# Kernel optimization log

Measured on AMD Instinct MI355X. Metric: run time of the kernel, lower is better.

## Reference

```python
import jax, jax.numpy as jnp
import numpy as np

E, H = 1024, 16


def setup_inputs() -> dict:
    key = jax.random.key(0)
    k1, k2, k3, k4 = jax.random.split(key, 4)
    B, L = 4, 2048
    embeddings = jax.random.normal(k1, (B, L, E), dtype=jnp.float32)
    mask = jax.random.randint(k2, (B, L, L), 0, 2) == 1  # True = masked out
    # Params (torch Linear y = x @ W.T; we store already-transposed [in, out])
    W_qkv = jax.random.normal(k3, (E, 3 * E), dtype=jnp.float32) * 0.02
    W_out = jax.random.normal(k4, (E, E), dtype=jnp.float32) * 0.02
    return {"embeddings": embeddings, "mask": mask, "W_qkv": W_qkv, "W_out": W_out}


def reference(embeddings, mask, W_qkv, W_out):
    B, L, E_ = embeddings.shape
    A = E_ // H
    scale = A ** (-0.5)
    qkv = embeddings @ W_qkv                       # [B, L, 3E]
    qkv = qkv.reshape(B, L, H, 3 * A).transpose(0, 2, 1, 3)  # [B, H, L, 3A]
    q, k, v = jnp.split(qkv, 3, axis=-1)           # each [B, H, L, A]
    scores = jnp.einsum('bhqa,bhka->bhqk', q, k) * scale  # [B, H, L, L]
    m = mask[:, None, :, :]                        # [B, 1, L, L]
    fully = jnp.all(m, axis=-1, keepdims=True)     # rows with every key masked
    scores = jnp.where(m, -jnp.inf, scores)
    scores = jnp.where(fully, 0.0, scores)         # keep softmax finite
    attn = jax.nn.softmax(scores, axis=-1)
    attn = jnp.where(fully, 0.0, attn)             # == torch nan_to_num(0)
    values = jnp.einsum('bhqk,bhka->bhqa', attn, v)  # [B, H, L, A]
    values = values.transpose(0, 2, 1, 3).reshape(B, L, E_)
    return values @ W_out
```

## Files before the change

kernel.cpp:

```cpp
#include <hip/hip_runtime.h>
#include <hip/hip_bf16.h>

#define B_   4
#define L_   2048
#define E_   1024
#define H_   16
#define T_   8192
#define K_   1024

typedef __attribute__((ext_vector_type(8))) short bf16x8;
typedef __attribute__((ext_vector_type(4))) float f32x4;
typedef __attribute__((ext_vector_type(4))) unsigned u32x4;

#define CSC_ (0.125f * 1.44269504f)

__device__ __forceinline__ ushort f2b(float f) {
    union { float f; unsigned u; } x; x.f = f;
    unsigned r = (x.u + 0x7fffu + ((x.u >> 16) & 1u)) >> 16;
    return (ushort)r;
}

__device__ __forceinline__ float fexp2(float x) {
#if __has_builtin(__builtin_amdgcn_exp2f)
    return __builtin_amdgcn_exp2f(x);
#else
    return __expf(x * 0.69314718056f);
#endif
}

__device__ __forceinline__ unsigned pack2bf(float a, float b) {
#if __has_builtin(__builtin_amdgcn_cvt_pk_bf16_f32)
    auto t = __builtin_amdgcn_cvt_pk_bf16_f32(a, b);
    return __builtin_bit_cast(unsigned, t);
#else
    unsigned ua = __builtin_bit_cast(unsigned, a) + 0x8000u;
    unsigned ub = __builtin_bit_cast(unsigned, b) + 0x8000u;
    return __builtin_amdgcn_perm(ub, ua, 0x07060302);
#endif
}

#define GLD_LDS16(gp, lp) __builtin_amdgcn_global_load_lds( \
    (const __attribute__((address_space(1))) void*)(gp), \
    (__attribute__((address_space(3))) void*)(lp), 16, 0, 0)

__global__ void detect_mask_layout(const unsigned char* __restrict__ m, int* flag) {
    __shared__ int s;
    if (threadIdx.x == 0) s = 0;
    __syncthreads();
    int found = 0;
    for (int i = threadIdx.x; i < 4096; i += 256)
        if ((i & 3) != 0 && m[i] != 0) found = 1;
    if (found) atomicOr(&s, 1);
    __syncthreads();
    if (threadIdx.x == 0) *flag = s;
}

__global__ void pack_mask(const void* __restrict__ mraw, const int* __restrict__ flag,
                          unsigned* __restrict__ tbits) {
    int row  = blockIdx.x;
    int lane = threadIdx.x & 63;
    int wave = threadIdx.x >> 6;
    int isByte = *flag;
    int b = row >> 11, q = row & 2047;
    const unsigned char* mb = (const unsigned char*)mraw;
    const int*           mi = (const int*)mraw;
    long long base = (long long)row * L_;
    for (int w = wave; w < 32; w += 4) {
        int idx = w * 64 + lane;
        int v = isByte ? (int)mb[base + idx] : mi[base + idx];
        unsigned long long word = __ballot(v == 0);
        if (lane == 0) {
            tbits[((size_t)b * 64 + 2 * w)     * 2048 + q] = (unsigned)word;
            tbits[((size_t)b * 64 + 2 * w + 1) * 2048 + q] = (unsigned)(word >> 32);
        }
    }
}

__global__ __launch_bounds__(256) void conv_bf16(const float* __restrict__ in,
                                                 ushort* __restrict__ out) {
    int i = blockIdx.x * 256 + threadIdx.x;
    float4 v = ((const float4*)in)[i];
    uint2 o;
    o.x = (unsigned)f2b(v.x) | ((unsigned)f2b(v.y) << 16);
    o.y = (unsigned)f2b(v.z) | ((unsigned)f2b(v.w) << 16);
    ((uint2*)out)[i] = o;
}

__global__ __launch_bounds__(256) void transpose_conv(const float* __restrict__ in,
        ushort* __restrict__ out, int R, int Cn) {
    __shared__ float t[32][33];
    int c0 = blockIdx.x * 32, r0 = blockIdx.y * 32;
    int x = threadIdx.x & 31, y = threadIdx.x >> 5;
#pragma unroll
    for (int k = 0; k < 4; ++k)
        t[y + k * 8][x] = in[(size_t)(r0 + y + k * 8) * Cn + c0 + x];
    __syncthreads();
#pragma unroll
    for (int k = 0; k < 4; ++k)
        out[(size_t)(c0 + y + k * 8) * R + r0 + x] = f2b(t[x][y + k * 8]);
}

template<int NDIM, int MODE>
__global__ __launch_bounds__(256) void gemm_bf16(
        const ushort* __restrict__ Ab, const ushort* __restrict__ Bt,
        float* __restrict__ Cg, ushort* __restrict__ Qb,
        ushort* __restrict__ Kb, ushort* __restrict__ Vt) {
    __shared__ ushort As[128 * 64];
    __shared__ ushort Bs[128 * 64];
    const int tid = threadIdx.x;
    const int wv = tid >> 6, ln = tid & 63;
    const int bn = blockIdx.x * 128, bm = blockIdx.y * 128;
    const int wm = (wv & 1) * 64, wn = (wv >> 1) * 64;
    const int row16 = ln & 15, quad = ln >> 4;
    const int cg8 = (((ln & 7) ^ (ln >> 3)) * 8);

    f32x4 acc[4][4];
#pragma unroll
    for (int i = 0; i < 4; ++i)
#pragma unroll
        for (int j = 0; j < 4; ++j) acc[i][j] = (f32x4){0.f, 0.f, 0.f, 0.f};

    for (int k0 = 0; k0 < K_; k0 += 64) {
        __syncthreads();
#pragma unroll
        for (int it = 0; it < 4; ++it) {
            int rA = wv * 32 + it * 8 + (ln >> 3);
            GLD_LDS16(Ab + (size_t)(bm + rA) * K_ + k0 + cg8, &As[(wv * 32 + it * 8) * 64]);
            GLD_LDS16(Bt + (size_t)(bn + rA) * K_ + k0 + cg8, &Bs[(wv * 32 + it * 8) * 64]);
        }
        __syncthreads();
#pragma unroll
        for (int ks = 0; ks < 2; ++ks) {
            const int ch = (((ks * 4 + quad) ^ (ln & 7)) * 8);
            bf16x8 af[4], bf[4];
#pragma unroll
            for (int i = 0; i < 4; ++i)
                af[i] = *(const bf16x8*)&As[(wm + i * 16 + row16) * 64 + ch];
#pragma unroll
            for (int j = 0; j < 4; ++j)
                bf[j] = *(const bf16x8*)&Bs[(wn + j * 16 + row16) * 64 + ch];
#pragma unroll
            for (int i = 0; i < 4; ++i)
#pragma unroll
                for (int j = 0; j < 4; ++j)
                    acc[i][j] = __builtin_amdgcn_mfma_f32_16x16x32_bf16(
                        af[i], bf[j], acc[i][j], 0, 0, 0);
        }
    }

    if (MODE == 0) {
#pragma unroll
        for (int i = 0; i < 4; ++i)
#pragma unroll
            for (int j = 0; j < 4; ++j) {
                int col = bn + wn + j * 16 + row16;
#pragma unroll
                for (int r = 0; r < 4; ++r) {
                    int row = bm + wm + i * 16 + quad * 4 + r;
                    Cg[(size_t)row * NDIM + col] = acc[i][j][r];
                }
            }
    } else {
#pragma unroll
        for (int j = 0; j < 4; ++j) {
            int col = bn + wn + j * 16 + row16;
            int h = col / 192, w = col - h * 192;
            int sel = w >> 6, a = w & 63;
            float qs = (sel == 0) ? CSC_ : 1.0f;
#pragma unroll
            for (int i = 0; i < 4; ++i)
#pragma unroll
                for (int r = 0; r < 4; ++r) {
                    int rowg = bm + wm + i * 16 + quad * 4 + r;
                    int b = rowg >> 11, l = rowg & 2047;
                    ushort v = f2b(acc[i][j][r] * qs);
                    size_t bh = (size_t)(b * H_ + h);
                    if (sel == 0)      Qb[(bh * L_ + l) * 64 + a] = v;
                    else if (sel == 1) Kb[(bh * L_ + l) * 64 + a] = v;
                    else {
                        int k5 = l & 31;
                        int lp = (l & ~31) | (2 * (k5 & 15) + (k5 >> 4));
                        Vt[(bh * 64 + a) * L_ + lp] = v;
                    }
                }
        }
    }
}

__global__ __launch_bounds__(512, 4) void attn_mfma(
        const ushort* __restrict__ Qb, const ushort* __restrict__ Kb,
        const ushort* __restrict__ Vt, const unsigned* __restrict__ tbits,
        ushort* __restrict__ vals) {
    __shared__ ushort KV[6][4096];

    const int tid = threadIdx.x, wv = tid >> 6, ln = tid & 63;
    const int bh = blockIdx.x, b = bh >> 4, h = bh & 15;
    const int q0 = blockIdx.y * 128;
    const int row16 = ln & 15, quad = ln >> 4;
    const int lh = ln >> 3, ll = ln & 7;
    const int cg8 = ((ll ^ lh) * 8);

    const ushort* Kg = Kb + (size_t)bh * L_ * 64;
    const ushort* Vg = Vt + (size_t)bh * 64 * L_;

    const int wk = wv & 3;
    const bool isK = (wv < 4);
    const int vc4 = ll ^ lh;
    const ushort* vstage = Vg + (size_t)(wk * 8 + lh + 32 * (vc4 >> 2)) * L_ + (vc4 & 3) * 8;
    const ushort* kstage = Kg + (size_t)(wk * 8 + lh) * 64 + cg8;

    {
        const ushort* Qgw = Qb + ((size_t)bh * L_ + q0 + wv * 16) * 64;
        GLD_LDS16(Qgw + (size_t)lh * 64 + cg8,       &KV[0][(wv * 16) * 64]);
        GLD_LDS16(Qgw + (size_t)(8 + lh) * 64 + cg8, &KV[0][(wv * 16 + 8) * 64]);
    }
    __syncthreads();
    bf16x8 aq[2];
#pragma unroll
    for (int ks = 0; ks < 2; ++ks)
        aq[ks] = *(const bf16x8*)&KV[0][(wv * 16 + row16) * 64 +
                                        (((ks * 4 + quad) ^ (row16 & 7)) * 8)];
    __syncthreads();

    if (isK) {
        GLD_LDS16(kstage,               &KV[0][(wk * 8) * 64]);
        GLD_LDS16(kstage + 2048,        &KV[0][(32 + wk * 8) * 64]);
        GLD_LDS16(kstage + 4096,        &KV[1][(wk * 8) * 64]);
        GLD_LDS16(kstage + 4096 + 2048, &KV[1][(32 + wk * 8) * 64]);
        kstage += 8192;
    } else {
        GLD_LDS16(vstage,      &KV[3][(wk * 8) * 64]);
        GLD_LDS16(vstage + 32, &KV[3][(32 + wk * 8) * 64]);
        GLD_LDS16(vstage + 64, &KV[4][(wk * 8) * 64]);
        GLD_LDS16(vstage + 96, &KV[4][(32 + wk * 8) * 64]);
        vstage += 128;
    }

    bf16x8 vone;
#pragma unroll
    for (int i = 0; i < 8; ++i) vone[i] = (short)0x3F80;
    const f32x4 zf = (f32x4){0.f, 0.f, 0.f, 0.f};

    f32x4 oacc[4], lacc = zf;
#pragma unroll
    for (int t = 0; t < 4; ++t) oacc[t] = zf;

    const unsigned* mptr = tbits + (size_t)b * 64 * 2048 + (q0 + wv * 16 + row16);

    auto qk = [&](const ushort* kbuf, int sub, f32x4 (&s)[2]) {
        __builtin_amdgcn_s_setprio(1);
#pragma unroll
        for (int ks = 0; ks < 2; ++ks) {
            bf16x8 bk[2];
#pragma unroll
            for (int t = 0; t < 2; ++t)
                bk[t] = *(const bf16x8*)&kbuf[(sub * 32 + t * 16 + row16) * 64 +
                                              (((ks * 4 + quad) ^ (row16 & 7)) * 8)];
#pragma unroll
            for (int t = 0; t < 2; ++t)
                s[t] = __builtin_amdgcn_mfma_f32_16x16x32_bf16(
                    bk[t], aq[ks], ks ? s[t] : zf, 0, 0, 0);
        }
        __builtin_amdgcn_s_setprio(0);
    };

    auto sm_pv = [&](f32x4 (&sa)[2], unsigned m, const ushort* vbuf, int sub) {
        u32x4 pw;
#pragma unroll
        for (int r = 0; r < 4; ++r) {
            unsigned sh = m >> (quad * 4 + r);
            unsigned pk = pack2bf(fexp2(sa[0][r]), fexp2(sa[1][r]));
            pk &= (sh & 0x00010001u) * 0xFFFFu;
            pw[r] = pk;
        }
        bf16x8 ap = __builtin_bit_cast(bf16x8, pw);
        bf16x8 bv[4];
#pragma unroll
        for (int t = 0; t < 4; ++t)
            bv[t] = *(const bf16x8*)&vbuf[(sub * 32 + (t & 1) * 16 + row16) * 64 +
                                          ((((t >> 1) * 4 + quad) ^ (row16 & 7)) * 8)];
        __builtin_amdgcn_s_setprio(1);
        lacc = __builtin_amdgcn_mfma_f32_16x16x32_bf16(ap, vone, lacc, 0, 0, 0);
#pragma unroll
        for (int t = 0; t < 4; ++t)
            oacc[t] = __builtin_amdgcn_mfma_f32_16x16x32_bf16(
                ap, bv[t], oacc[t], 0, 0, 0);
        __builtin_amdgcn_s_setprio(0);
    };

    auto iter = [&](const ushort* kb, const ushort* vb,
                    ushort* kn, ushort* vn, bool st) {
        unsigned m0 = mptr[0], m1 = mptr[2048];
        mptr += 4096;
        __builtin_amdgcn_sched_barrier(0);
        if (st) {
            if (isK) {
                GLD_LDS16(kstage,        kn + (wk * 8) * 64);
                GLD_LDS16(kstage + 2048, kn + (32 + wk * 8) * 64);
                kstage += 4096;
            } else {
                GLD_LDS16(vstage,      vn + (wk * 8) * 64);
                GLD_LDS16(vstage + 32, vn + (32 + wk * 8) * 64);
                vstage += 64;
            }
        }
        f32x4 s0[2], s1[2];
        qk(kb, 0, s0);
        qk(kb, 1, s1);
        sm_pv(s0, m0, vb, 0);
        sm_pv(s1, m1, vb, 1);
        asm volatile("s_waitcnt vmcnt(2)" ::: "memory");
        __builtin_amdgcn_s_barrier();
        __builtin_amdgcn_sched_barrier(0);
    };

    asm volatile("s_waitcnt vmcnt(2)" ::: "memory");
    __builtin_amdgcn_s_barrier();
    __builtin_amdgcn_sched_barrier(0);

    for (int g = 0; g < 10; ++g) {
        iter(KV[0], KV[3], KV[2], KV[5], true);
        iter(KV[1], KV[4], KV[0], KV[3], true);
        iter(KV[2], KV[5], KV[1], KV[4], true);
    }
    iter(KV[0], KV[3], KV[2], KV[5], false);
    iter(KV[1], KV[4], KV[0], KV[3], false);

#pragma unroll
    for (int r = 0; r < 4; ++r) {
        float l = lacc[r];
        float inv = (l > 0.f) ? 1.0f / l : 0.f;
        int qrow = q0 + wv * 16 + quad * 4 + r;
        size_t base = ((size_t)b * L_ + qrow) * E_ + h * 64;
#pragma unroll
        for (int t = 0; t < 4; ++t)
            vals[base + t * 16 + row16] = f2b(oacc[t][r] * inv);
    }
}

extern "C" void kernel_launch(void* const* d_in, const int* in_sizes, int n_in,
                              void* d_out, int out_size, void* d_ws, size_t ws_size,
                              hipStream_t stream) {
    const float* emb  = (const float*)d_in[0];
    const void*  mask = d_in[1];
    const float* wqkv = (const float*)d_in[2];
    const float* wout = (const float*)d_in[3];
    float* out = (float*)d_out;

    char* ws = (char*)d_ws;
    const size_t NEED = 4096ull + 2097152ull + 2ull * 46137344ull;
    if (ws_size < NEED) return;

    int* flag = (int*)ws;
    unsigned* tbits = (unsigned*)(ws + 4096);
    ushort* embb  = (ushort*)(ws + 4096 + 2097152);
    ushort* Wqkvt = embb  + 8388608;
    ushort* Wott  = Wqkvt + 3145728;
    ushort* Qb    = Wott  + 1048576;
    ushort* Kb    = Qb    + 8388608;
    ushort* Vt    = Kb    + 8388608;
    ushort* vals  = Vt    + 8388608;

    detect_mask_layout<<<1, 256, 0, stream>>>((const unsigned char*)mask, flag);
    pack_mask<<<T_, 256, 0, stream>>>(mask, flag, tbits);
    conv_bf16<<<8192, 256, 0, stream>>>(emb, embb);
    transpose_conv<<<dim3(96, 32), 256, 0, stream>>>(wqkv, Wqkvt, 1024, 3072);
    transpose_conv<<<dim3(32, 32), 256, 0, stream>>>(wout, Wott, 1024, 1024);
    gemm_bf16<3072, 1><<<dim3(24, 64), 256, 0, stream>>>(
        embb, Wqkvt, nullptr, Qb, Kb, Vt);
    attn_mfma<<<dim3(64, 16), 512, 0, stream>>>(Qb, Kb, Vt, tbits, vals);
    gemm_bf16<1024, 0><<<dim3(8, 64), 256, 0, stream>>>(
        vals, Wott, out, nullptr, nullptr, nullptr);
}
```

Measured before the change: 355.6 us.

## Process two 16-row query groups per wave to reuse K/V fragments

```diff
diff --git a/kernel.cpp b/kernel.cpp
--- a/kernel.cpp
+++ b/kernel.cpp
@@ -195,7 +195,7 @@
 
     const int tid = threadIdx.x, wv = tid >> 6, ln = tid & 63;
     const int bh = blockIdx.x, b = bh >> 4, h = bh & 15;
-    const int q0 = blockIdx.y * 128;
+    const int q0 = blockIdx.y * 256;
     const int row16 = ln & 15, quad = ln >> 4;
     const int lh = ln >> 3, ll = ln & 7;
     const int cg8 = ((ll ^ lh) * 8);
@@ -209,17 +209,23 @@
     const ushort* vstage = Vg + (size_t)(wk * 8 + lh + 32 * (vc4 >> 2)) * L_ + (vc4 & 3) * 8;
     const ushort* kstage = Kg + (size_t)(wk * 8 + lh) * 64 + cg8;
 
+    ushort* lds = &KV[0][0];
+
     {
-        const ushort* Qgw = Qb + ((size_t)bh * L_ + q0 + wv * 16) * 64;
-        GLD_LDS16(Qgw + (size_t)lh * 64 + cg8,       &KV[0][(wv * 16) * 64]);
-        GLD_LDS16(Qgw + (size_t)(8 + lh) * 64 + cg8, &KV[0][(wv * 16 + 8) * 64]);
+        const ushort* Qgw = Qb + ((size_t)bh * L_ + q0 + wv * 32) * 64;
+#pragma unroll
+        for (int it = 0; it < 4; ++it)
+            GLD_LDS16(Qgw + (size_t)(it * 8 + lh) * 64 + cg8,
+                      lds + (wv * 32 + it * 8) * 64);
     }
     __syncthreads();
-    bf16x8 aq[2];
-#pragma unroll
-    for (int ks = 0; ks < 2; ++ks)
-        aq[ks] = *(const bf16x8*)&KV[0][(wv * 16 + row16) * 64 +
-                                        (((ks * 4 + quad) ^ (row16 & 7)) * 8)];
+    bf16x8 aq[2][2];
+#pragma unroll
+    for (int rg = 0; rg < 2; ++rg)
+#pragma unroll
+        for (int ks = 0; ks < 2; ++ks)
+            aq[rg][ks] = *(const bf16x8*)&lds[(wv * 32 + rg * 16 + row16) * 64 +
+                                              (((ks * 4 + quad) ^ (row16 & 7)) * 8)];
     __syncthreads();
 
     if (isK) {
@@ -241,13 +247,17 @@
     for (int i = 0; i < 8; ++i) vone[i] = (short)0x3F80;
     const f32x4 zf = (f32x4){0.f, 0.f, 0.f, 0.f};
 
-    f32x4 oacc[4], lacc = zf;
-#pragma unroll
-    for (int t = 0; t < 4; ++t) oacc[t] = zf;
-
-    const unsigned* mptr = tbits + (size_t)b * 64 * 2048 + (q0 + wv * 16 + row16);
-
-    auto qk = [&](const ushort* kbuf, int sub, f32x4 (&s)[2]) {
+    f32x4 oacc[2][4], lacc[2];
+#pragma unroll
+    for (int rg = 0; rg < 2; ++rg) {
+        lacc[rg] = zf;
+#pragma unroll
+        for (int t = 0; t < 4; ++t) oacc[rg][t] = zf;
+    }
+
+    const unsigned* mptr = tbits + (size_t)b * 64 * 2048 + (q0 + wv * 32 + row16);
+
+    auto qk = [&](const ushort* kbuf, int sub, f32x4 (&s)[2][2]) {
         __builtin_amdgcn_s_setprio(1);
 #pragma unroll
         for (int ks = 0; ks < 2; ++ks) {
@@ -257,40 +267,53 @@
                 bk[t] = *(const bf16x8*)&kbuf[(sub * 32 + t * 16 + row16) * 64 +
                                               (((ks * 4 + quad) ^ (row16 & 7)) * 8)];
 #pragma unroll
-            for (int t = 0; t < 2; ++t)
-                s[t] = __builtin_amdgcn_mfma_f32_16x16x32_bf16(
-                    bk[t], aq[ks], ks ? s[t] : zf, 0, 0, 0);
+            for (int rg = 0; rg < 2; ++rg)
+#pragma unroll
+                for (int t = 0; t < 2; ++t)
+                    s[rg][t] = __builtin_amdgcn_mfma_f32_16x16x32_bf16(
+                        bk[t], aq[rg][ks], ks ? s[rg][t] : zf, 0, 0, 0);
         }
         __builtin_amdgcn_s_setprio(0);
     };
 
-    auto sm_pv = [&](f32x4 (&sa)[2], unsigned m, const ushort* vbuf, int sub) {
-        u32x4 pw;
-#pragma unroll
-        for (int r = 0; r < 4; ++r) {
-            unsigned sh = m >> (quad * 4 + r);
-            unsigned pk = pack2bf(fexp2(sa[0][r]), fexp2(sa[1][r]));
-            pk &= (sh & 0x00010001u) * 0xFFFFu;
-            pw[r] = pk;
-        }
-        bf16x8 ap = __builtin_bit_cast(bf16x8, pw);
+    auto sm_pv = [&](f32x4 (&sa)[2][2], unsigned mlo, unsigned mhi,
+                     const ushort* vbuf, int sub) {
+        bf16x8 ap[2];
+#pragma unroll
+        for (int rg = 0; rg < 2; ++rg) {
+            unsigned wr = rg ? mhi : mlo;
+            u32x4 pw;
+#pragma unroll
+            for (int r = 0; r < 4; ++r) {
+                unsigned sh = wr >> (quad * 4 + r);
+                unsigned pk = pack2bf(fexp2(sa[rg][0][r]), fexp2(sa[rg][1][r]));
+                pk &= (sh & 0x00010001u) * 0xFFFFu;
+                pw[r] = pk;
+            }
+            ap[rg] = __builtin_bit_cast(bf16x8, pw);
+        }
         bf16x8 bv[4];
 #pragma unroll
         for (int t = 0; t < 4; ++t)
             bv[t] = *(const bf16x8*)&vbuf[(sub * 32 + (t & 1) * 16 + row16) * 64 +
                                           ((((t >> 1) * 4 + quad) ^ (row16 & 7)) * 8)];
         __builtin_amdgcn_s_setprio(1);
-        lacc = __builtin_amdgcn_mfma_f32_16x16x32_bf16(ap, vone, lacc, 0, 0, 0);
-#pragma unroll
-        for (int t = 0; t < 4; ++t)
-            oacc[t] = __builtin_amdgcn_mfma_f32_16x16x32_bf16(
-                ap, bv[t], oacc[t], 0, 0, 0);
+#pragma unroll
+        for (int rg = 0; rg < 2; ++rg) {
+            lacc[rg] = __builtin_amdgcn_mfma_f32_16x16x32_bf16(
+                ap[rg], vone, lacc[rg], 0, 0, 0);
+#pragma unroll
+            for (int t = 0; t < 4; ++t)
+                oacc[rg][t] = __builtin_amdgcn_mfma_f32_16x16x32_bf16(
+                    ap[rg], bv[t], oacc[rg][t], 0, 0, 0);
+        }
         __builtin_amdgcn_s_setprio(0);
     };
 
     auto iter = [&](const ushort* kb, const ushort* vb,
                     ushort* kn, ushort* vn, bool st) {
-        unsigned m0 = mptr[0], m1 = mptr[2048];
+        unsigned m0lo = mptr[0],    m0hi = mptr[16];
+        unsigned m1lo = mptr[2048], m1hi = mptr[2048 + 16];
         mptr += 4096;
         __builtin_amdgcn_sched_barrier(0);
         if (st) {
@@ -304,11 +327,12 @@
                 vstage += 64;
             }
         }
-        f32x4 s0[2], s1[2];
+        f32x4 s0[2][2];
         qk(kb, 0, s0);
+        sm_pv(s0, m0lo, m0hi, vb, 0);
+        f32x4 s1[2][2];
         qk(kb, 1, s1);
-        sm_pv(s0, m0, vb, 0);
-        sm_pv(s1, m1, vb, 1);
+        sm_pv(s1, m1lo, m1hi, vb, 1);
         asm volatile("s_waitcnt vmcnt(2)" ::: "memory");
         __builtin_amdgcn_s_barrier();
         __builtin_amdgcn_sched_barrier(0);
@@ -327,15 +351,17 @@
     iter(KV[1], KV[4], KV[0], KV[3], false);
 
 #pragma unroll
-    for (int r = 0; r < 4; ++r) {
-        float l = lacc[r];
-        float inv = (l > 0.f) ? 1.0f / l : 0.f;
-        int qrow = q0 + wv * 16 + quad * 4 + r;
-        size_t base = ((size_t)b * L_ + qrow) * E_ + h * 64;
-#pragma unroll
-        for (int t = 0; t < 4; ++t)
-            vals[base + t * 16 + row16] = f2b(oacc[t][r] * inv);
-    }
+    for (int rg = 0; rg < 2; ++rg)
+#pragma unroll
+        for (int r = 0; r < 4; ++r) {
+            float l = lacc[rg][r];
+            float inv = (l > 0.f) ? 1.0f / l : 0.f;
+            int qrow = q0 + wv * 32 + rg * 16 + quad * 4 + r;
+            size_t base = ((size_t)b * L_ + qrow) * E_ + h * 64;
+#pragma unroll
+            for (int t = 0; t < 4; ++t)
+                vals[base + t * 16 + row16] = f2b(oacc[rg][t][r] * inv);
+        }
 }
 
 extern "C" void kernel_launch(void* const* d_in, const int* in_sizes, int n_in,
@@ -368,7 +394,7 @@
     transpose_conv<<<dim3(32, 32), 256, 0, stream>>>(wout, Wott, 1024, 1024);
     gemm_bf16<3072, 1><<<dim3(24, 64), 256, 0, stream>>>(
         embb, Wqkvt, nullptr, Qb, Kb, Vt);
-    attn_mfma<<<dim3(64, 16), 512, 0, stream>>>(Qb, Kb, Vt, tbits, vals);
+    attn_mfma<<<dim3(64, 8), 512, 0, stream>>>(Qb, Kb, Vt, tbits, vals);
     gemm_bf16<1024, 0><<<dim3(8, 64), 256, 0, stream>>>(
         vals, Wott, out, nullptr, nullptr, nullptr);
 }
```

Measured after the change: 357.1 us. Within noise of the previous version (+0.4%).
